# Optimization experiments

Measured on AMD Instinct MI355X. Metric: run time of the kernel, lower is better.

Reference implementation:

```python
import jax, jax.numpy as jnp
import numpy as np

B, S, D, H, NL = 4, 1024, 512, 8, 2
DFF = 4 * D
EPS = 1e-5


def _layernorm(x, g, b):
    m = x.mean(-1, keepdims=True)
    v = ((x - m) ** 2).mean(-1, keepdims=True)
    return (x - m) / jnp.sqrt(v + EPS) * g + b


def _forward(x, Wq, bq, Wk, bk, Wv, bv, Wo, bo, W1, b1, W2, b2, ln1_g, ln1_b, ln2_g, ln2_b):
    Bn, Sn, Dn = x.shape
    Nl, Hh = Wq.shape[0], Wq.shape[1]
    dk = Dn // Hh  # scaling uses dmodel//h even though heads are full-width (faithful to SDPA)
    for i in range(Nl):
        # per-head full-width projections: each head maps dmodel -> dmodel
        q = jnp.einsum('bsd,hed->bhse', x, Wq[i]) + bq[i][:, None, :]
        k = jnp.einsum('bsd,hed->bhse', x, Wk[i]) + bk[i][:, None, :]
        v = jnp.einsum('bsd,hed->bhse', x, Wv[i]) + bv[i][:, None, :]
        scores = jnp.einsum('bhse,bhte->bhst', q, k) / jnp.sqrt(jnp.asarray(dk, x.dtype))
        attn = jax.nn.softmax(scores, axis=-1)
        heads = jnp.einsum('bhst,bhte->bhse', attn, v)          # [B,H,S,D]
        cat = heads.transpose(0, 2, 1, 3).reshape(Bn, Sn, Hh * Dn)  # concat heads -> [B,S,H*D]
        mha_out = cat @ Wo[i].T + bo[i]
        x = _layernorm(x + mha_out, ln1_g[i], ln1_b[i])
        ff = jax.nn.relu(x @ W1[i].T + b1[i]) @ W2[i].T + b2[i]
        x = _layernorm(x + ff, ln2_g[i], ln2_b[i])
    return x


def setup_inputs() -> dict:
    key = jax.random.key(0)
    ks = jax.random.split(key, 12)
    def w(k, shape, fan_in):
        return (jax.random.normal(k, shape, jnp.float32) / np.sqrt(fan_in)).astype(jnp.float32)
    inp = {
        'x': jax.random.normal(ks[0], (B, S, D), jnp.float32),
        'Wq': w(ks[1], (NL, H, D, D), D), 'bq': jnp.zeros((NL, H, D), jnp.float32),
        'Wk': w(ks[2], (NL, H, D, D), D), 'bk': jnp.zeros((NL, H, D), jnp.float32),
        'Wv': w(ks[3], (NL, H, D, D), D), 'bv': jnp.zeros((NL, H, D), jnp.float32),
        'Wo': w(ks[4], (NL, D, H * D), H * D), 'bo': jnp.zeros((NL, D), jnp.float32),
        'W1': w(ks[5], (NL, DFF, D), D), 'b1': jnp.zeros((NL, DFF), jnp.float32),
        'W2': w(ks[6], (NL, D, DFF), DFF), 'b2': jnp.zeros((NL, D), jnp.float32),
        'ln1_g': jnp.ones((NL, D), jnp.float32), 'ln1_b': jnp.zeros((NL, D), jnp.float32),
        'ln2_g': jnp.ones((NL, D), jnp.float32), 'ln2_b': jnp.zeros((NL, D), jnp.float32),
    }
    return inp


def reference(x, Wq, bq, Wk, bk, Wv, bv, Wo, bo, W1, b1, W2, b2, ln1_g, ln1_b, ln2_g, ln2_b):
    return _forward(x, Wq, bq, Wk, bk, Wv, bv, Wo, bo, W1, b1, W2, b2, ln1_g, ln1_b, ln2_g, ln2_b)
```

## Files before the change

kernel.cpp:

```cpp
#include <hip/hip_runtime.h>
#include <cstdint>
#include <cstddef>

#define NB 4
#define NS 1024
#define ND 512
#define NH 8
#define NLAYER 2
#define NDFF 2048

typedef __attribute__((ext_vector_type(8))) short short8;
typedef __attribute__((ext_vector_type(4))) float f32x4;
typedef __attribute__((ext_vector_type(4))) unsigned short u16x4;
typedef unsigned short u16;
typedef long long ll;

__device__ __forceinline__ float b2f(u16 u) {
  union { unsigned int i; float f; } x; x.i = ((unsigned int)u) << 16; return x.f;
}
__device__ __forceinline__ u16 f2b(float f) {
  union { float f; unsigned int i; } x; x.f = f;
  return (u16)((x.i + 0x7FFF + ((x.i >> 16) & 1)) >> 16);
}

struct Zm { int div; ll hi, lo; };
__device__ __forceinline__ ll zoff(Zm m, int z) {
  return (ll)(z / m.div) * m.hi + (ll)(z % m.div) * m.lo;
}

enum { F_BF16 = 1, F_RELU = 2, F_BCOL = 4, F_BROW = 8, F_RESID = 16 };

__device__ __forceinline__ void load_lds16(const void* g, void* s) {
  __builtin_amdgcn_global_load_lds(
      (const __attribute__((address_space(1))) void*)(uintptr_t)g,
      (__attribute__((address_space(3))) void*)(uint32_t)(uintptr_t)s, 16, 0, 0);
}

__global__ void __launch_bounds__(256)
gemm_bt(const u16* __restrict__ A, int lda, Zm za,
        const u16* __restrict__ Bw, int ldb, Zm zb,
        void* __restrict__ Cv, int ldc, Zm zc,
        const float* __restrict__ bias, Zm zbias,
        const float* __restrict__ resid,
        float scale, int K, int flags)
{
  __shared__ __align__(16) u16 lA[128 * 32];
  __shared__ __align__(16) u16 lB[128 * 32];

  const int z = blockIdx.z;
  A  += zoff(za, z);
  Bw += zoff(zb, z);
  const int bm = blockIdx.y * 128, bn = blockIdx.x * 128;
  const int t = threadIdx.x;
  const int w = t >> 6, lane = t & 63;
  const int wr = w >> 1, wc = w & 1;

  const u16* ga0 = A  + (size_t)(bm + (t >> 2)) * lda + ((t & 3) << 3);
  const u16* ga1 = ga0 + (size_t)64 * lda;
  const u16* gb0 = Bw + (size_t)(bn + (t >> 2)) * ldb + ((t & 3) << 3);
  const u16* gb1 = gb0 + (size_t)64 * ldb;
  char* sa = (char*)lA + (w << 10);
  char* sb = (char*)lB + (w << 10);

  f32x4 acc[4][4];
#pragma unroll
  for (int i = 0; i < 4; ++i)
#pragma unroll
    for (int j = 0; j < 4; ++j) acc[i][j] = (f32x4){0.f, 0.f, 0.f, 0.f};

  const int fr = lane & 15;
  const int kg = (lane >> 4) << 3;

  for (int k0 = 0; k0 < K; k0 += 32) {
    load_lds16(ga0 + k0, sa);
    load_lds16(ga1 + k0, sa + 4096);
    load_lds16(gb0 + k0, sb);
    load_lds16(gb1 + k0, sb + 4096);
    __syncthreads();
    short8 af[4], bf[4];
#pragma unroll
    for (int mi = 0; mi < 4; ++mi)
      af[mi] = *(const short8*)(lA + (wr * 64 + mi * 16 + fr) * 32 + kg);
#pragma unroll
    for (int ni = 0; ni < 4; ++ni)
      bf[ni] = *(const short8*)(lB + (wc * 64 + ni * 16 + fr) * 32 + kg);
#pragma unroll
    for (int mi = 0; mi < 4; ++mi)
#pragma unroll
      for (int ni = 0; ni < 4; ++ni)
        asm volatile("v_mfma_f32_16x16x32_bf16 %0, %1, %2, %0"
                     : "+v"(acc[mi][ni]) : "v"(af[mi]), "v"(bf[ni]));
    __syncthreads();
  }

  asm volatile("s_nop 7\n\ts_nop 7" ::: "memory");

  const ll co = zoff(zc, z);
  const float* bz = (flags & (F_BCOL | F_BROW)) ? bias + zoff(zbias, z) : nullptr;
  const int r0 = (lane >> 4) << 2;
  const int c0 = lane & 15;
#pragma unroll
  for (int mi = 0; mi < 4; ++mi) {
#pragma unroll
    for (int ni = 0; ni < 4; ++ni) {
#pragma unroll
      for (int r = 0; r < 4; ++r) {
        const int grow = bm + wr * 64 + mi * 16 + r0 + r;
        const int gcol = bn + wc * 64 + ni * 16 + c0;
        float v = acc[mi][ni][r] * scale;
        if (flags & F_BCOL) v += bz[gcol];
        if (flags & F_BROW) v += bz[grow];
        if (flags & F_RELU) v = fmaxf(v, 0.f);
        if (flags & F_RESID) v += resid[(size_t)grow * ldc + gcol];
        const ll idx = co + (ll)grow * ldc + gcol;
        if (flags & F_BF16) ((u16*)Cv)[idx] = f2b(v);
        else                ((float*)Cv)[idx] = v;
      }
    }
  }
}

__global__ void __launch_bounds__(256)
softmax_rows(u16* __restrict__ sc)
{
  const int row = blockIdx.x;
  u16* p = sc + (size_t)row * 1024;
  const int t = threadIdx.x;
  const int w = t >> 6, lane = t & 63;
  u16x4 u = *(const u16x4*)(p + t * 4);
  float v0 = b2f(u.x), v1 = b2f(u.y), v2 = b2f(u.z), v3 = b2f(u.w);
  float mx = fmaxf(fmaxf(v0, v1), fmaxf(v2, v3));
#pragma unroll
  for (int o = 32; o >= 1; o >>= 1) mx = fmaxf(mx, __shfl_xor(mx, o));
  __shared__ float red[8];
  if (lane == 0) red[w] = mx;
  __syncthreads();
  mx = fmaxf(fmaxf(red[0], red[1]), fmaxf(red[2], red[3]));
  float e0 = __expf(v0 - mx), e1 = __expf(v1 - mx);
  float e2 = __expf(v2 - mx), e3 = __expf(v3 - mx);
  float s = e0 + e1 + e2 + e3;
#pragma unroll
  for (int o = 32; o >= 1; o >>= 1) s += __shfl_xor(s, o);
  if (lane == 0) red[4 + w] = s;
  __syncthreads();
  s = red[4] + red[5] + red[6] + red[7];
  const float inv = 1.f / s;
  u16x4 o4;
  o4.x = f2b(e0 * inv); o4.y = f2b(e1 * inv);
  o4.z = f2b(e2 * inv); o4.w = f2b(e3 * inv);
  *(u16x4*)(p + t * 4) = o4;
}

__global__ void __launch_bounds__(64)
ln_red(const float* __restrict__ parts, int np, ll pstride,
       const float* __restrict__ bias, const float* __restrict__ resid,
       const float* __restrict__ g, const float* __restrict__ be,
       float* __restrict__ xout, u16* __restrict__ xbout)
{
  const int row = blockIdx.x;
  const int t = threadIdx.x;
  const ll base = (ll)row * ND + t * 8;
  float v[8];
  *(f32x4*)(v)     = *(const f32x4*)(resid + base);
  *(f32x4*)(v + 4) = *(const f32x4*)(resid + base + 4);
#pragma unroll
  for (int j = 0; j < 8; ++j) v[j] += bias[t * 8 + j];
  for (int pIdx = 0; pIdx < np; ++pIdx) {
    const float* pp = parts + pIdx * pstride + base;
    f32x4 a0 = *(const f32x4*)(pp);
    f32x4 a1 = *(const f32x4*)(pp + 4);
    v[0] += a0.x; v[1] += a0.y; v[2] += a0.z; v[3] += a0.w;
    v[4] += a1.x; v[5] += a1.y; v[6] += a1.z; v[7] += a1.w;
  }
  float s = 0.f, q = 0.f;
#pragma unroll
  for (int j = 0; j < 8; ++j) { s += v[j]; q += v[j] * v[j]; }
#pragma unroll
  for (int o = 32; o >= 1; o >>= 1) { s += __shfl_xor(s, o); q += __shfl_xor(q, o); }
  const float mean = s * (1.f / ND);
  const float var  = q * (1.f / ND) - mean * mean;
  const float inv  = 1.f / sqrtf(var + 1e-5f);
#pragma unroll
  for (int j = 0; j < 8; ++j) {
    const int c = t * 8 + j;
    const float y = (v[j] - mean) * inv * g[c] + be[c];
    xout[(ll)row * ND + c] = y;
    xbout[(ll)row * ND + c] = f2b(y);
  }
}

struct CvtJobs { const float* src[6]; u16* dst[6]; ll n[6]; };

__global__ void __launch_bounds__(256)
cvt6(CvtJobs j)
{
  const int z = blockIdx.y;
  const ll i = ((ll)blockIdx.x * 256 + threadIdx.x) * 4;
  if (i >= j.n[z]) return;
  f32x4 v = *(const f32x4*)(j.src[z] + i);
  u16x4 o;
  o.x = f2b(v.x); o.y = f2b(v.y); o.z = f2b(v.z); o.w = f2b(v.w);
  *(u16x4*)(j.dst[z] + i) = o;
}

__global__ void __launch_bounds__(256)
f32_to_bf16(const float* __restrict__ in, u16* __restrict__ out, ll n)
{
  const ll i = ((ll)blockIdx.x * 256 + threadIdx.x) * 4;
  if (i >= n) return;
  f32x4 v = *(const f32x4*)(in + i);
  u16x4 o;
  o.x = f2b(v.x); o.y = f2b(v.y); o.z = f2b(v.z); o.w = f2b(v.w);
  *(u16x4*)(out + i) = o;
}

extern "C" void kernel_launch(void* const* d_in, const int* in_sizes, int n_in,
                              void* d_out, int out_size, void* d_ws, size_t ws_size,
                              hipStream_t stream)
{
  (void)in_sizes; (void)n_in; (void)out_size; (void)ws_size;
  const float* x_in = (const float*)d_in[0];
  const float* Wq = (const float*)d_in[1];  const float* bq = (const float*)d_in[2];
  const float* Wk = (const float*)d_in[3];  const float* bk = (const float*)d_in[4];
  const float* Wv = (const float*)d_in[5];  const float* bv = (const float*)d_in[6];
  const float* Wo = (const float*)d_in[7];  const float* bo = (const float*)d_in[8];
  const float* W1 = (const float*)d_in[9];  const float* b1 = (const float*)d_in[10];
  const float* W2 = (const float*)d_in[11]; const float* b2 = (const float*)d_in[12];
  const float* ln1g = (const float*)d_in[13]; const float* ln1b = (const float*)d_in[14];
  const float* ln2g = (const float*)d_in[15]; const float* ln2b = (const float*)d_in[16];

  char* p = (char*)d_ws;
  auto alloc = [&](ll bytes) { char* r = p; p += (bytes + 255) & ~(ll)255; return r; };
  const ll nWq = (ll)NLAYER * NH * ND * ND;
  const ll nWo = (ll)NLAYER * ND * NH * ND;
  const ll nW1 = (ll)NLAYER * NDFF * ND;
  const ll nX  = (ll)NB * NS * ND;

  u16* wq_b = (u16*)alloc(nWq * 2);
  u16* wk_b = (u16*)alloc(nWq * 2);
  u16* wv_b = (u16*)alloc(nWq * 2);
  u16* wo_b = (u16*)alloc(nWo * 2);
  u16* w1_b = (u16*)alloc(nW1 * 2);
  u16* w2_b = (u16*)alloc(nW1 * 2);
  u16* xb   = (u16*)alloc(nX * 2);
  u16* qb   = (u16*)alloc((ll)NH * NB * NS * ND * 2);
  u16* kb   = (u16*)alloc((ll)NH * NB * NS * ND * 2);
  u16* vT   = (u16*)alloc((ll)NH * NB * ND * NS * 2);
  u16* scb  = (u16*)alloc((ll)NB * NH * NS * NS * 2);
  u16* cat = kb;
  u16* ffh = qb;
  float* parts = (float*)scb;

  CvtJobs cj;
  cj.src[0] = Wq; cj.dst[0] = wq_b; cj.n[0] = nWq;
  cj.src[1] = Wk; cj.dst[1] = wk_b; cj.n[1] = nWq;
  cj.src[2] = Wv; cj.dst[2] = wv_b; cj.n[2] = nWq;
  cj.src[3] = Wo; cj.dst[3] = wo_b; cj.n[3] = nWo;
  cj.src[4] = W1; cj.dst[4] = w1_b; cj.n[4] = nW1;
  cj.src[5] = W2; cj.dst[5] = w2_b; cj.n[5] = nW1;
  cvt6<<<dim3((unsigned)((nWq / 4 + 255) / 256), 6), 256, 0, stream>>>(cj);
  f32_to_bf16<<<dim3((unsigned)((nX / 4 + 255) / 256)), 256, 0, stream>>>(x_in, xb, nX);

  float* xf = (float*)d_out;
  const Zm Z0{1, 0, 0};
  const ll PSTR = (ll)NB * NS * ND;

  for (int i = 0; i < NLAYER; ++i) {
    const float* resid1 = (i == 0) ? x_in : xf;
    const ll woff = (ll)i * NH * ND * ND;

    gemm_bt<<<dim3(ND/128, (NB*NS)/128, NH), 256, 0, stream>>>(
        xb, ND, Z0, wq_b + woff, ND, Zm{1, (ll)ND * ND, 0},
        qb, ND, Zm{1, (ll)NB * NS * ND, 0},
        bq + (ll)i * NH * ND, Zm{1, ND, 0}, nullptr, 1.f, ND, F_BF16 | F_BCOL);
    gemm_bt<<<dim3(ND/128, (NB*NS)/128, NH), 256, 0, stream>>>(
        xb, ND, Z0, wk_b + woff, ND, Zm{1, (ll)ND * ND, 0},
        kb, ND, Zm{1, (ll)NB * NS * ND, 0},
        bk + (ll)i * NH * ND, Zm{1, ND, 0}, nullptr, 1.f, ND, F_BF16 | F_BCOL);

    gemm_bt<<<dim3(NS/128, ND/128, NH*NB), 256, 0, stream>>>(
        wv_b + woff, ND, Zm{NB, (ll)ND * ND, 0},
        xb, ND, Zm{NB, 0, (ll)NS * ND},
        vT, NS, Zm{1, (ll)ND * NS, 0},
        bv + (ll)i * NH * ND, Zm{NB, ND, 0}, nullptr, 1.f, ND, F_BF16 | F_BROW);

    gemm_bt<<<dim3(NS/128, NS/128, NH*NB), 256, 0, stream>>>(
        qb, ND, Zm{NB, (ll)NB * NS * ND, (ll)NS * ND},
        kb, ND, Zm{NB, (ll)NB * NS * ND, (ll)NS * ND},
        scb, NS, Zm{1, (ll)NS * NS, 0},
        nullptr, Z0, nullptr, 0.125f, ND, F_BF16);

    softmax_rows<<<dim3(NB * NH * NS), 256, 0, stream>>>(scb);

    gemm_bt<<<dim3(ND/128, NS/128, NH*NB), 256, 0, stream>>>(
        scb, NS, Zm{1, (ll)NS * NS, 0},
        vT, NS, Zm{1, (ll)ND * NS, 0},
        cat, NH * ND, Zm{NB, (ll)ND, (ll)NS * NH * ND},
        nullptr, Z0, nullptr, 1.f, NS, F_BF16);

    gemm_bt<<<dim3(ND/128, (NB*NS)/128, 8), 256, 0, stream>>>(
        cat, NH * ND, Zm{1, 512, 0},
        wo_b + (ll)i * ND * NH * ND, NH * ND, Zm{1, 512, 0},
        parts, ND, Zm{1, PSTR, 0},
        nullptr, Z0, nullptr, 1.f, 512, 0);

    ln_red<<<dim3(NB * NS), 64, 0, stream>>>(
        parts, 8, PSTR, bo + (ll)i * ND, resid1,
        ln1g + (ll)i * ND, ln1b + (ll)i * ND, xf, xb);

    gemm_bt<<<dim3(NDFF/128, (NB*NS)/128, 1), 256, 0, stream>>>(
        xb, ND, Z0,
        w1_b + (ll)i * NDFF * ND, ND, Z0,
        ffh, NDFF, Z0,
        b1 + (ll)i * NDFF, Z0, nullptr, 1.f, ND, F_BF16 | F_BCOL | F_RELU);

    gemm_bt<<<dim3(ND/128, (NB*NS)/128, 4), 256, 0, stream>>>(
        ffh, NDFF, Zm{1, 512, 0},
        w2_b + (ll)i * ND * NDFF, NDFF, Zm{1, 512, 0},
        parts, ND, Zm{1, PSTR, 0},
        nullptr, Z0, nullptr, 1.f, 512, 0);

    ln_red<<<dim3(NB * NS), 64, 0, stream>>>(
        parts, 4, PSTR, b2 + (ll)i * ND, xf,
        ln2g + (ll)i * ND, ln2b + (ll)i * ND, xf, xb);
  }
}
```

Before: 800.4 us.

## Double-buffer GEMM LDS, remap workgroups across XCDs, merge Q/K launches, wave-per-row softmax/LN

The GEMM kernel now double-buffers its LDS tiles so the next K-slice loads while the current one is computed, halving barriers per iteration. It also remaps workgroup IDs so consecutive blocks are spread across the eight XCDs. Q and K projections are merged into one launch through a z-split second weight and bias. Softmax and layernorm switch to one wavefront per row with 4 rows per block, which drops the LDS reductions, and the x conversion is folded into the weight conversion kernel. Together these cut launch count and sync overhead, at the cost of doubled LDS per block and a possible loss of L2 locality from the remapping.

```diff
diff --git a/kernel.cpp b/kernel.cpp
--- a/kernel.cpp
+++ b/kernel.cpp
@@ -39,51 +39,75 @@
 __global__ void __launch_bounds__(256)
 gemm_bt(const u16* __restrict__ A, int lda, Zm za,
         const u16* __restrict__ Bw, int ldb, Zm zb,
+        const u16* __restrict__ Bw2, const float* __restrict__ bias2, int zsplit,
         void* __restrict__ Cv, int ldc, Zm zc,
         const float* __restrict__ bias, Zm zbias,
         const float* __restrict__ resid,
         float scale, int K, int flags)
 {
-  __shared__ __align__(16) u16 lA[128 * 32];
-  __shared__ __align__(16) u16 lB[128 * 32];
-
-  const int z = blockIdx.z;
-  A  += zoff(za, z);
-  Bw += zoff(zb, z);
-  const int bm = blockIdx.y * 128, bn = blockIdx.x * 128;
+  __shared__ __align__(16) char smem[2][16384];
+
+  const int gx = gridDim.x, gy = gridDim.y;
+  int id = (blockIdx.z * gy + blockIdx.y) * gx + blockIdx.x;
+  const int nwg = gx * gy * (int)gridDim.z;
+  if ((nwg & 7) == 0) id = (id & 7) * (nwg >> 3) + (id >> 3);
+  const int bx = id % gx;
+  const int rest = id / gx;
+  const int by = rest % gy;
+  const int z0 = rest / gy;
+
+  int zB = z0;
+  const u16* Bsel = Bw;
+  const float* bsel = bias;
+  if (z0 >= zsplit) { Bsel = Bw2; bsel = bias2; zB = z0 - zsplit; }
+
+  A    += zoff(za, z0);
+  Bsel += zoff(zb, zB);
+
+  const int bm = by * 128, bn = bx * 128;
   const int t = threadIdx.x;
   const int w = t >> 6, lane = t & 63;
   const int wr = w >> 1, wc = w & 1;
 
-  const u16* ga0 = A  + (size_t)(bm + (t >> 2)) * lda + ((t & 3) << 3);
+  const u16* ga0 = A    + (size_t)(bm + (t >> 2)) * lda + ((t & 3) << 3);
   const u16* ga1 = ga0 + (size_t)64 * lda;
-  const u16* gb0 = Bw + (size_t)(bn + (t >> 2)) * ldb + ((t & 3) << 3);
+  const u16* gb0 = Bsel + (size_t)(bn + (t >> 2)) * ldb + ((t & 3) << 3);
   const u16* gb1 = gb0 + (size_t)64 * ldb;
-  char* sa = (char*)lA + (w << 10);
-  char* sb = (char*)lB + (w << 10);
-
-  f32x4 acc[4][4];
-#pragma unroll
-  for (int i = 0; i < 4; ++i)
-#pragma unroll
-    for (int j = 0; j < 4; ++j) acc[i][j] = (f32x4){0.f, 0.f, 0.f, 0.f};
-
-  const int fr = lane & 15;
-  const int kg = (lane >> 4) << 3;
-
-  for (int k0 = 0; k0 < K; k0 += 32) {
+
+  auto STAGE = [&](int sel, int kt) {
+    const int k0 = kt << 5;
+    char* sa = smem[sel] + (w << 10);
+    char* sb = smem[sel] + 8192 + (w << 10);
     load_lds16(ga0 + k0, sa);
     load_lds16(ga1 + k0, sa + 4096);
     load_lds16(gb0 + k0, sb);
     load_lds16(gb1 + k0, sb + 4096);
-    __syncthreads();
+  };
+
+  f32x4 acc[4][4];
+#pragma unroll
+  for (int i = 0; i < 4; ++i)
+#pragma unroll
+    for (int j = 0; j < 4; ++j) acc[i][j] = (f32x4){0.f, 0.f, 0.f, 0.f};
+
+  const int fr = lane & 15;
+  const int kg = (lane >> 4) << 3;
+
+  const int nt = K >> 5;
+  STAGE(0, 0);
+  __syncthreads();
+  int cur = 0;
+  for (int kt = 0; kt < nt; ++kt) {
+    if (kt + 1 < nt) STAGE(cur ^ 1, kt + 1);
+    const u16* la = (const u16*)smem[cur];
+    const u16* lb = (const u16*)(smem[cur] + 8192);
     short8 af[4], bf[4];
 #pragma unroll
     for (int mi = 0; mi < 4; ++mi)
-      af[mi] = *(const short8*)(lA + (wr * 64 + mi * 16 + fr) * 32 + kg);
+      af[mi] = *(const short8*)(la + (wr * 64 + mi * 16 + fr) * 32 + kg);
 #pragma unroll
     for (int ni = 0; ni < 4; ++ni)
-      bf[ni] = *(const short8*)(lB + (wc * 64 + ni * 16 + fr) * 32 + kg);
+      bf[ni] = *(const short8*)(lb + (wc * 64 + ni * 16 + fr) * 32 + kg);
 #pragma unroll
     for (int mi = 0; mi < 4; ++mi)
 #pragma unroll
@@ -91,12 +115,13 @@
         asm volatile("v_mfma_f32_16x16x32_bf16 %0, %1, %2, %0"
                      : "+v"(acc[mi][ni]) : "v"(af[mi]), "v"(bf[ni]));
     __syncthreads();
+    cur ^= 1;
   }
 
   asm volatile("s_nop 7\n\ts_nop 7" ::: "memory");
 
-  const ll co = zoff(zc, z);
-  const float* bz = (flags & (F_BCOL | F_BROW)) ? bias + zoff(zbias, z) : nullptr;
+  const ll co = zoff(zc, z0);
+  const float* bz = (flags & (F_BCOL | F_BROW)) ? bsel + zoff(zbias, zB) : nullptr;
   const int r0 = (lane >> 4) << 2;
   const int c0 = lane & 15;
 #pragma unroll
@@ -123,48 +148,48 @@
 __global__ void __launch_bounds__(256)
 softmax_rows(u16* __restrict__ sc)
 {
-  const int row = blockIdx.x;
-  u16* p = sc + (size_t)row * 1024;
-  const int t = threadIdx.x;
-  const int w = t >> 6, lane = t & 63;
-  u16x4 u = *(const u16x4*)(p + t * 4);
-  float v0 = b2f(u.x), v1 = b2f(u.y), v2 = b2f(u.z), v3 = b2f(u.w);
-  float mx = fmaxf(fmaxf(v0, v1), fmaxf(v2, v3));
+  const int t = threadIdx.x, w = t >> 6, lane = t & 63;
+  u16* p = sc + ((ll)blockIdx.x * 4 + w) * 1024 + lane * 16;
+  short8 a = *(const short8*)p;
+  short8 b = *(const short8*)(p + 8);
+  float v[16];
+#pragma unroll
+  for (int j = 0; j < 8; ++j) { v[j] = b2f((u16)a[j]); v[8 + j] = b2f((u16)b[j]); }
+  float mx = v[0];
+#pragma unroll
+  for (int j = 1; j < 16; ++j) mx = fmaxf(mx, v[j]);
 #pragma unroll
   for (int o = 32; o >= 1; o >>= 1) mx = fmaxf(mx, __shfl_xor(mx, o));
-  __shared__ float red[8];
-  if (lane == 0) red[w] = mx;
-  __syncthreads();
-  mx = fmaxf(fmaxf(red[0], red[1]), fmaxf(red[2], red[3]));
-  float e0 = __expf(v0 - mx), e1 = __expf(v1 - mx);
-  float e2 = __expf(v2 - mx), e3 = __expf(v3 - mx);
-  float s = e0 + e1 + e2 + e3;
+  float s = 0.f;
+#pragma unroll
+  for (int j = 0; j < 16; ++j) { v[j] = __expf(v[j] - mx); s += v[j]; }
 #pragma unroll
   for (int o = 32; o >= 1; o >>= 1) s += __shfl_xor(s, o);
-  if (lane == 0) red[4 + w] = s;
-  __syncthreads();
-  s = red[4] + red[5] + red[6] + red[7];
   const float inv = 1.f / s;
-  u16x4 o4;
-  o4.x = f2b(e0 * inv); o4.y = f2b(e1 * inv);
-  o4.z = f2b(e2 * inv); o4.w = f2b(e3 * inv);
-  *(u16x4*)(p + t * 4) = o4;
-}
-
-__global__ void __launch_bounds__(64)
+  short8 oa, ob;
+#pragma unroll
+  for (int j = 0; j < 8; ++j) {
+    oa[j] = (short)f2b(v[j] * inv);
+    ob[j] = (short)f2b(v[8 + j] * inv);
+  }
+  *(short8*)p = oa;
+  *(short8*)(p + 8) = ob;
+}
+
+__global__ void __launch_bounds__(256)
 ln_red(const float* __restrict__ parts, int np, ll pstride,
        const float* __restrict__ bias, const float* __restrict__ resid,
        const float* __restrict__ g, const float* __restrict__ be,
        float* __restrict__ xout, u16* __restrict__ xbout)
 {
-  const int row = blockIdx.x;
-  const int t = threadIdx.x;
-  const ll base = (ll)row * ND + t * 8;
+  const int t = threadIdx.x, w = t >> 6, lane = t & 63;
+  const ll row = (ll)blockIdx.x * 4 + w;
+  const ll base = row * ND + lane * 8;
   float v[8];
   *(f32x4*)(v)     = *(const f32x4*)(resid + base);
   *(f32x4*)(v + 4) = *(const f32x4*)(resid + base + 4);
 #pragma unroll
-  for (int j = 0; j < 8; ++j) v[j] += bias[t * 8 + j];
+  for (int j = 0; j < 8; ++j) v[j] += bias[lane * 8 + j];
   for (int pIdx = 0; pIdx < np; ++pIdx) {
     const float* pp = parts + pIdx * pstride + base;
     f32x4 a0 = *(const f32x4*)(pp);
@@ -182,17 +207,17 @@
   const float inv  = 1.f / sqrtf(var + 1e-5f);
 #pragma unroll
   for (int j = 0; j < 8; ++j) {
-    const int c = t * 8 + j;
+    const int c = lane * 8 + j;
     const float y = (v[j] - mean) * inv * g[c] + be[c];
-    xout[(ll)row * ND + c] = y;
-    xbout[(ll)row * ND + c] = f2b(y);
-  }
-}
-
-struct CvtJobs { const float* src[6]; u16* dst[6]; ll n[6]; };
+    xout[row * ND + c] = y;
+    xbout[row * ND + c] = f2b(y);
+  }
+}
+
+struct CvtJobs { const float* src[7]; u16* dst[7]; ll n[7]; };
 
 __global__ void __launch_bounds__(256)
-cvt6(CvtJobs j)
+cvt7(CvtJobs j)
 {
   const int z = blockIdx.y;
   const ll i = ((ll)blockIdx.x * 256 + threadIdx.x) * 4;
@@ -201,17 +226,6 @@
   u16x4 o;
   o.x = f2b(v.x); o.y = f2b(v.y); o.z = f2b(v.z); o.w = f2b(v.w);
   *(u16x4*)(j.dst[z] + i) = o;
-}
-
-__global__ void __launch_bounds__(256)
-f32_to_bf16(const float* __restrict__ in, u16* __restrict__ out, ll n)
-{
-  const ll i = ((ll)blockIdx.x * 256 + threadIdx.x) * 4;
-  if (i >= n) return;
-  f32x4 v = *(const f32x4*)(in + i);
-  u16x4 o;
-  o.x = f2b(v.x); o.y = f2b(v.y); o.z = f2b(v.z); o.w = f2b(v.w);
-  *(u16x4*)(out + i) = o;
 }
 
 extern "C" void kernel_launch(void* const* d_in, const int* in_sizes, int n_in,
@@ -258,69 +272,74 @@
   cj.src[3] = Wo; cj.dst[3] = wo_b; cj.n[3] = nWo;
   cj.src[4] = W1; cj.dst[4] = w1_b; cj.n[4] = nW1;
   cj.src[5] = W2; cj.dst[5] = w2_b; cj.n[5] = nW1;
-  cvt6<<<dim3((unsigned)((nWq / 4 + 255) / 256), 6), 256, 0, stream>>>(cj);
-  f32_to_bf16<<<dim3((unsigned)((nX / 4 + 255) / 256)), 256, 0, stream>>>(x_in, xb, nX);
+  cj.src[6] = x_in; cj.dst[6] = xb; cj.n[6] = nX;
+  cvt7<<<dim3((unsigned)((nWq / 4 + 255) / 256), 7), 256, 0, stream>>>(cj);
 
   float* xf = (float*)d_out;
   const Zm Z0{1, 0, 0};
   const ll PSTR = (ll)NB * NS * ND;
+  const int ZINF = 1 << 30;
 
   for (int i = 0; i < NLAYER; ++i) {
     const float* resid1 = (i == 0) ? x_in : xf;
     const ll woff = (ll)i * NH * ND * ND;
 
-    gemm_bt<<<dim3(ND/128, (NB*NS)/128, NH), 256, 0, stream>>>(
-        xb, ND, Z0, wq_b + woff, ND, Zm{1, (ll)ND * ND, 0},
+    gemm_bt<<<dim3(ND/128, (NB*NS)/128, 2*NH), 256, 0, stream>>>(
+        xb, ND, Z0,
+        wq_b + woff, ND, Zm{1, (ll)ND * ND, 0},
+        wk_b + woff, bk + (ll)i * NH * ND, NH,
         qb, ND, Zm{1, (ll)NB * NS * ND, 0},
         bq + (ll)i * NH * ND, Zm{1, ND, 0}, nullptr, 1.f, ND, F_BF16 | F_BCOL);
-    gemm_bt<<<dim3(ND/128, (NB*NS)/128, NH), 256, 0, stream>>>(
-        xb, ND, Z0, wk_b + woff, ND, Zm{1, (ll)ND * ND, 0},
-        kb, ND, Zm{1, (ll)NB * NS * ND, 0},
-        bk + (ll)i * NH * ND, Zm{1, ND, 0}, nullptr, 1.f, ND, F_BF16 | F_BCOL);
 
     gemm_bt<<<dim3(NS/128, ND/128, NH*NB), 256, 0, stream>>>(
         wv_b + woff, ND, Zm{NB, (ll)ND * ND, 0},
         xb, ND, Zm{NB, 0, (ll)NS * ND},
+        xb, nullptr, ZINF,
         vT, NS, Zm{1, (ll)ND * NS, 0},
         bv + (ll)i * NH * ND, Zm{NB, ND, 0}, nullptr, 1.f, ND, F_BF16 | F_BROW);
 
     gemm_bt<<<dim3(NS/128, NS/128, NH*NB), 256, 0, stream>>>(
         qb, ND, Zm{NB, (ll)NB * NS * ND, (ll)NS * ND},
         kb, ND, Zm{NB, (ll)NB * NS * ND, (ll)NS * ND},
+        kb, nullptr, ZINF,
         scb, NS, Zm{1, (ll)NS * NS, 0},
         nullptr, Z0, nullptr, 0.125f, ND, F_BF16);
 
-    softmax_rows<<<dim3(NB * NH * NS), 256, 0, stream>>>(scb);
+    softmax_rows<<<dim3(NB * NH * NS / 4), 256, 0, stream>>>(scb);
 
     gemm_bt<<<dim3(ND/128, NS/128, NH*NB), 256, 0, stream>>>(
         scb, NS, Zm{1, (ll)NS * NS, 0},
         vT, NS, Zm{1, (ll)ND * NS, 0},
+        vT, nullptr, ZINF,
         cat, NH * ND, Zm{NB, (ll)ND, (ll)NS * NH * ND},
         nullptr, Z0, nullptr, 1.f, NS, F_BF16);
 
     gemm_bt<<<dim3(ND/128, (NB*NS)/128, 8), 256, 0, stream>>>(
         cat, NH * ND, Zm{1, 512, 0},
         wo_b + (ll)i * ND * NH * ND, NH * ND, Zm{1, 512, 0},
+        wo_b, nullptr, ZINF,
         parts, ND, Zm{1, PSTR, 0},
         nullptr, Z0, nullptr, 1.f, 512, 0);
 
-    ln_red<<<dim3(NB * NS), 64, 0, stream>>>(
+    ln_red<<<dim3(NB * NS / 4), 256, 0, stream>>>(
         parts, 8, PSTR, bo + (ll)i * ND, resid1,
         ln1g + (ll)i * ND, ln1b + (ll)i * ND, xf, xb);
 
     gemm_bt<<<dim3(NDFF/128, (NB*NS)/128, 1), 256, 0, stream>>>(
         xb, ND, Z0,
         w1_b + (ll)i * NDFF * ND, ND, Z0,
+        w1_b, nullptr, ZINF,
         ffh, NDFF, Z0,
         b1 + (ll)i * NDFF, Z0, nullptr, 1.f, ND, F_BF16 | F_BCOL | F_RELU);
 
     gemm_bt<<<dim3(ND/128, (NB*NS)/128, 4), 256, 0, stream>>>(
         ffh, NDFF, Zm{1, 512, 0},
         w2_b + (ll)i * ND * NDFF, NDFF, Zm{1, 512, 0},
+        w2_b, nullptr, ZINF,
         parts, ND, Zm{1, PSTR, 0},
         nullptr, Z0, nullptr, 1.f, 512, 0);
 
-    ln_red<<<dim3(NB * NS), 64, 0, stream>>>(
+    ln_red<<<dim3(NB * NS / 4), 256, 0, stream>>>(
         parts, 4, PSTR, b2 + (ll)i * ND, xf,
         ln2g + (ll)i * ND, ln2b + (ll)i * ND, xf, xb);
   }
```

Measured after the change: 681.6 us. -14.8%, faster.
